# Performance work log

Measured on AMD Instinct MI355X. Metric: run time of the kernel, lower is better.

The kernel has to match this reference:

```python
import jax, jax.numpy as jnp
import numpy as np

DIM = 1024
HEADS = 16
HEAD_DIM = DIM // HEADS
D_FF = 4 * DIM
EPS = 1e-5


def _layernorm(x, g, b):
    mu = jnp.mean(x, axis=-1, keepdims=True)
    var = jnp.mean(jnp.square(x - mu), axis=-1, keepdims=True)
    return (x - mu) * jax.lax.rsqrt(var + EPS) * g + b


def setup_inputs() -> dict:
    key = jax.random.key(0)
    ks = jax.random.split(key, 8)
    s = 0.02
    return {
        "x": jax.random.normal(ks[0], (2, 2048, DIM), dtype=jnp.float32),
        "Wqkv": jax.random.normal(ks[1], (DIM, 3 * DIM), dtype=jnp.float32) * s,
        "bqkv": jnp.zeros((3 * DIM,), dtype=jnp.float32),
        "Wout": jax.random.normal(ks[2], (DIM, DIM), dtype=jnp.float32) * s,
        "bout": jnp.zeros((DIM,), dtype=jnp.float32),
        "W1": jax.random.normal(ks[3], (DIM, D_FF), dtype=jnp.float32) * s,
        "b1": jnp.zeros((D_FF,), dtype=jnp.float32),
        "W2": jax.random.normal(ks[4], (D_FF, DIM), dtype=jnp.float32) * s,
        "b2": jnp.zeros((DIM,), dtype=jnp.float32),
        "g1": jnp.ones((DIM,), dtype=jnp.float32),
        "be1": jnp.zeros((DIM,), dtype=jnp.float32),
        "g2": jnp.ones((DIM,), dtype=jnp.float32),
        "be2": jnp.zeros((DIM,), dtype=jnp.float32),
    }


def reference(x, Wqkv, bqkv, Wout, bout, W1, b1, W2, b2, g1, be1, g2, be2):
    B, T, C = x.shape
    # --- multi-head self-attention (explicit QK^T softmax, no mask/cache) ---
    qkv = (x @ Wqkv + bqkv).reshape(B, T, 3, HEADS, HEAD_DIM)
    q = qkv[:, :, 0].transpose(0, 2, 1, 3)  # (B,H,T,hd)
    k = qkv[:, :, 1].transpose(0, 2, 1, 3)
    v = qkv[:, :, 2].transpose(0, 2, 1, 3)
    scale = HEAD_DIM ** -0.5
    scores = jnp.einsum("bhqd,bhkd->bhqk", q, k) * scale  # (B,H,T,T)
    attn = jax.nn.softmax(scores, axis=-1)
    o = jnp.einsum("bhqk,bhkd->bhqd", attn, v)
    o = o.transpose(0, 2, 1, 3).reshape(B, T, C)
    attn_out = o @ Wout + bout
    # --- Post-LN: LN applied to sublayer output, then residual ---
    x = x + _layernorm(attn_out, g1, be1)
    # --- FFN with exact GELU ---
    h = jax.nn.gelu(x @ W1 + b1, approximate=False)
    ffn_out = h @ W2 + b2
    x = x + _layernorm(ffn_out, g2, be2)
    return x
```

## Files before the change

kernel.cpp:

```cpp
#include <hip/hip_runtime.h>
#include <cstdint>
#include <cstddef>

#define DIM 1024
#define HEADS 16
#define HD 64
#define DFF 4096
#define TSEQ 2048
#define EPS 1e-5f

#define WAITCNT_VM4 0xF74
#define WAITCNT_VM0 0xF70
#define WAITCNT_VM8 0xF78
#define WAITCNT_VM4_LGKM0 0x074
#define WAITCNT_VM0_LGKM0 0x070

typedef __bf16 bf16x8 __attribute__((ext_vector_type(8)));
typedef float floatx4 __attribute__((ext_vector_type(4)));

__device__ __forceinline__ unsigned short f2bf(float f) {
  union { float f; unsigned int u; } v; v.f = f;
  return (unsigned short)((v.u + 0x7FFFu + ((v.u >> 16) & 1u)) >> 16);
}

__device__ __forceinline__ float gelu_f(float v) {
  const float u = v * (0.7978845608f + 0.0356774081f * v * v);
  const float e = __expf(2.0f * u);
  const float t = 1.0f - 2.0f / (e + 1.0f);
  return 0.5f * v * (1.0f + t);
}

__device__ __forceinline__ void async16(const void* g, void* l) {
  __builtin_amdgcn_global_load_lds(
      (const __attribute__((address_space(1))) void*)g,
      (__attribute__((address_space(3))) void*)l, 16, 0, 0);
}

__global__ __launch_bounds__(256) void prep_all(const float* __restrict__ x,
                                                const float* __restrict__ Wqkv,
                                                const float* __restrict__ Wout,
                                                const float* __restrict__ W1,
                                                const float* __restrict__ W2,
                                                unsigned short* __restrict__ xb,
                                                unsigned short* __restrict__ WqkvT,
                                                unsigned short* __restrict__ WoutT,
                                                unsigned short* __restrict__ W1T,
                                                unsigned short* __restrict__ W2T) {
  const int bid = blockIdx.x;
  const int tid = threadIdx.x;
  if (bid < 4096) {
    const int i = bid * 256 + tid;
    float4 v = ((const float4*)x)[i];
    ushort4 o;
    o.x = f2bf(v.x); o.y = f2bf(v.y); o.z = f2bf(v.z); o.w = f2bf(v.w);
    ((ushort4*)xb)[i] = o;
    return;
  }
  int id = bid - 4096;
  const float* src; unsigned short* dst; int R, C, gx;
  if (id < 3072)      {            src = Wqkv; dst = WqkvT; R = 1024; C = 3072; gx = 96; }
  else if (id < 4096) { id -= 3072; src = Wout; dst = WoutT; R = 1024; C = 1024; gx = 32; }
  else if (id < 8192) { id -= 4096; src = W1;   dst = W1T;   R = 1024; C = 4096; gx = 128; }
  else                { id -= 8192; src = W2;   dst = W2T;   R = 4096; C = 1024; gx = 32; }
  const int c0 = (id % gx) * 32, r0 = (id / gx) * 32;
  const int tx = tid & 31, ty = tid >> 5;
  __shared__ float tile[32][33];
#pragma unroll
  for (int i = 0; i < 32; i += 8)
    tile[ty + i][tx] = src[(size_t)(r0 + ty + i) * C + c0 + tx];
  __syncthreads();
#pragma unroll
  for (int i = 0; i < 32; i += 8)
    dst[(size_t)(c0 + ty + i) * R + r0 + tx] = f2bf(tile[tx][ty + i]);
}

#define PIPELINED_KLOOP(NIT, STRIDE_EXPR)                                           \
  auto issue = [&](int s, int k0) {                                                  \
    async16(Ab0 + k0, &lds[s][tid * 8]);                                             \
    async16(Ab1 + k0, &lds[s][2048 + tid * 8]);                                      \
    async16(Bb0 + k0, &lds[s][4096 + tid * 8]);                                      \
    async16(Bb1 + k0, &lds[s][6144 + tid * 8]);                                      \
  };                                                                                 \
  issue(0, 0);                                                                       \
  issue(1, 32);                                                                      \
  int sidx = 0;                                                                      \
  for (int k = 0; k < (NIT); k++) {                                                  \
    if (k < (NIT)-1) __builtin_amdgcn_s_waitcnt(WAITCNT_VM4);                        \
    else             __builtin_amdgcn_s_waitcnt(WAITCNT_VM0);                        \
    __builtin_amdgcn_s_barrier();                                                    \
    if (k + 2 < (NIT)) {                                                             \
      int s2 = sidx + 2; if (s2 >= 3) s2 -= 3;                                       \
      issue(s2, (k + 2) * 32);                                                       \
    }                                                                                \
    bf16x8 af[4], bg[4];                                                             \
    _Pragma("unroll")                                                                \
    for (int mi = 0; mi < 4; mi++)                                                   \
      af[mi] = *(const bf16x8*)&lds[sidx][(wm + mi * 16 + l16) * 32 + quad * 8];     \
    _Pragma("unroll")                                                                \
    for (int ni = 0; ni < 4; ni++)                                                   \
      bg[ni] = *(const bf16x8*)&lds[sidx][4096 + (wn + ni * 16 + l16) * 32 + quad * 8]; \
    _Pragma("unroll")                                                                \
    for (int mi = 0; mi < 4; mi++)                                                   \
      _Pragma("unroll")                                                              \
      for (int ni = 0; ni < 4; ni++)                                                 \
        acc[mi][ni] =                                                                \
            __builtin_amdgcn_mfma_f32_16x16x32_bf16(af[mi], bg[ni], acc[mi][ni], 0, 0, 0); \
    sidx = (sidx == 2) ? 0 : sidx + 1;                                               \
  }

template <int EPI>
__global__ __launch_bounds__(256) void gemm_bt(const unsigned short* __restrict__ A,
                                               const unsigned short* __restrict__ Bt,
                                               const float* __restrict__ bias,
                                               void* __restrict__ Cout,
                                               int M, int N, int K) {
  __shared__ unsigned short lds[3][8192];
  const int tid = threadIdx.x;
  const int bm = blockIdx.y * 128, bn = blockIdx.x * 128;
  const int wave = tid >> 6, lane = tid & 63;
  const int l16 = lane & 15, quad = lane >> 4;
  const int wm = (wave >> 1) * 64, wn = (wave & 1) * 64;

  floatx4 acc[4][4] = {};

  const int srow = tid >> 2;
  const int scol = (tid & 3) * 8;

  const unsigned short* Ab0 = A + (size_t)(bm + srow) * K + scol;
  const unsigned short* Ab1 = A + (size_t)(bm + 64 + srow) * K + scol;
  const unsigned short* Bb0 = Bt + (size_t)(bn + srow) * K + scol;
  const unsigned short* Bb1 = Bt + (size_t)(bn + 64 + srow) * K + scol;

  const int nit = K >> 5;
  PIPELINED_KLOOP(nit, 32)
  __syncthreads();

  if (EPI == 0) {
#pragma unroll
    for (int ni = 0; ni < 4; ni++) {
      const int col = bn + wn + ni * 16 + l16;
      const float bv = bias[col];
#pragma unroll
      for (int mi = 0; mi < 4; mi++) {
        const int row0 = bm + wm + mi * 16 + quad * 4;
#pragma unroll
        for (int r = 0; r < 4; r++)
          ((float*)Cout)[(size_t)(row0 + r) * N + col] = acc[mi][ni][r] + bv;
      }
    }
  } else {
    unsigned short* eb = &lds[0][wave * 1152];
    float bvv[4];
#pragma unroll
    for (int ni = 0; ni < 4; ni++) bvv[ni] = bias[bn + wn + ni * 16 + l16];
    const int lrow = lane >> 2, ck = lane & 3;
#pragma unroll
    for (int mi = 0; mi < 4; mi++) {
#pragma unroll
      for (int ni = 0; ni < 4; ni++)
#pragma unroll
        for (int r = 0; r < 4; r++)
          eb[(quad * 4 + r) * 72 + ni * 16 + l16] =
              f2bf(gelu_f(acc[mi][ni][r] + bvv[ni]));
      __syncthreads();
      unsigned short* gp =
          (unsigned short*)Cout + (size_t)(bm + wm + mi * 16 + lrow) * N + bn + wn;
#pragma unroll
      for (int j = 0; j < 2; j++)
        *(uint4*)(gp + j * 32 + ck * 8) = *(const uint4*)&eb[lrow * 72 + j * 32 + ck * 8];
      __syncthreads();
    }
  }
}

__global__ __launch_bounds__(256) void gemm_splitk(const unsigned short* __restrict__ A,
                                                   const unsigned short* __restrict__ Bt,
                                                   float* __restrict__ Cp,
                                                   int M, int N, int Ktot, int Ksl) {
  __shared__ unsigned short lds[3][8192];
  const int tid = threadIdx.x;
  const int bm = blockIdx.y * 128, bn = blockIdx.x * 128;
  const int koff = blockIdx.z * Ksl;
  const int wave = tid >> 6, lane = tid & 63;
  const int l16 = lane & 15, quad = lane >> 4;
  const int wm = (wave >> 1) * 64, wn = (wave & 1) * 64;

  floatx4 acc[4][4] = {};

  const int srow = tid >> 2;
  const int scol = (tid & 3) * 8;

  const unsigned short* Ab0 = A + (size_t)(bm + srow) * Ktot + koff + scol;
  const unsigned short* Ab1 = A + (size_t)(bm + 64 + srow) * Ktot + koff + scol;
  const unsigned short* Bb0 = Bt + (size_t)(bn + srow) * Ktot + koff + scol;
  const unsigned short* Bb1 = Bt + (size_t)(bn + 64 + srow) * Ktot + koff + scol;

  const int nit = Ksl >> 5;
  PIPELINED_KLOOP(nit, 32)

  float* out = Cp + (size_t)blockIdx.z * M * (size_t)N;
#pragma unroll
  for (int ni = 0; ni < 4; ni++) {
    const int col = bn + wn + ni * 16 + l16;
#pragma unroll
    for (int mi = 0; mi < 4; mi++) {
      const int row0 = bm + wm + mi * 16 + quad * 4;
#pragma unroll
      for (int r = 0; r < 4; r++)
        out[(size_t)(row0 + r) * N + col] = acc[mi][ni][r];
    }
  }
}

__global__ __launch_bounds__(256) void gemm_qkv(const unsigned short* __restrict__ A,
                                                const unsigned short* __restrict__ Bt,
                                                const float* __restrict__ bias,
                                                unsigned short* __restrict__ Qg,
                                                unsigned short* __restrict__ Kg,
                                                unsigned short* __restrict__ Vtg) {
  const int K = 1024;
  __shared__ unsigned short lds[3][8192];
  const int tid = threadIdx.x;
  const int bm = blockIdx.y * 128, bn = blockIdx.x * 128;
  const int wave = tid >> 6, lane = tid & 63;
  const int l16 = lane & 15, quad = lane >> 4;
  const int wm = (wave >> 1) * 64, wn = (wave & 1) * 64;

  floatx4 acc[4][4] = {};

  const int srow = tid >> 2;
  const int scol = (tid & 3) * 8;

  const unsigned short* Ab0 = A + (size_t)(bm + srow) * K + scol;
  const unsigned short* Ab1 = A + (size_t)(bm + 64 + srow) * K + scol;
  const unsigned short* Bb0 = Bt + (size_t)(bn + srow) * K + scol;
  const unsigned short* Bb1 = Bt + (size_t)(bn + 64 + srow) * K + scol;

  const int nit = K >> 5;
  PIPELINED_KLOOP(nit, 32)

#pragma unroll
  for (int ni = 0; ni < 4; ni++) {
    const int col = bn + wn + ni * 16 + l16;
    const float bv = bias[col];
    const int sec = col >> 10;
    const int cc = col & 1023;
    const int hh = cc >> 6, dd = cc & 63;
#pragma unroll
    for (int mi = 0; mi < 4; mi++) {
      const int row0 = bm + wm + mi * 16 + quad * 4;
      const int b2 = row0 >> 11, tt0 = row0 & 2047;
      if (sec == 0) {
        unsigned short* q = Qg + ((size_t)(b2 * HEADS + hh) * TSEQ + tt0) * HD + dd;
#pragma unroll
        for (int r = 0; r < 4; r++)
          q[(size_t)r * HD] = f2bf((acc[mi][ni][r] + bv) * 0.125f);
      } else if (sec == 1) {
        unsigned short* k = Kg + ((size_t)(b2 * HEADS + hh) * TSEQ + tt0) * HD + dd;
#pragma unroll
        for (int r = 0; r < 4; r++)
          k[(size_t)r * HD] = f2bf(acc[mi][ni][r] + bv);
      } else {
        ushort4 o;
        o.x = f2bf(acc[mi][ni][0] + bv);
        o.y = f2bf(acc[mi][ni][1] + bv);
        o.z = f2bf(acc[mi][ni][2] + bv);
        o.w = f2bf(acc[mi][ni][3] + bv);
        *(ushort4*)(Vtg + ((size_t)(b2 * HEADS + hh) * HD + dd) * TSEQ + tt0) = o;
      }
    }
  }
}

__global__ __launch_bounds__(256) void attn_mfma(const unsigned short* __restrict__ Qg,
                                                 const unsigned short* __restrict__ Kg,
                                                 const unsigned short* __restrict__ Vtg,
                                                 unsigned short* __restrict__ ob) {
  __shared__ unsigned short QPs[128 * 64];
  __shared__ unsigned short Ks[3][64 * 64];
  __shared__ unsigned short Vs[3][64 * 64];
  const int qt = blockIdx.x, h = blockIdx.y, b = blockIdx.z;
  const int tid = threadIdx.x;
  const int w = tid >> 6, lane = tid & 63, l16 = lane & 15, quad = lane >> 4;

  const int r0 = tid >> 3;
  const int c0 = (tid & 7) ^ (r0 & 7);

  const char* Qbase = (const char*)(Qg + ((size_t)(b * HEADS + h) * TSEQ + qt * 128) * HD);
  const char* Kbase = (const char*)(Kg + (size_t)(b * HEADS + h) * TSEQ * HD);
  const char* Vbase = (const char*)(Vtg + (size_t)(b * HEADS + h) * HD * TSEQ);

  auto issueKV = [&](int s, int ch) {
    const size_t koff = (size_t)ch * 64;
#pragma unroll
    for (int i = 0; i < 2; i++) {
      async16(Kbase + (koff + r0 + i * 32) * 128 + c0 * 16,
              (char*)Ks[s] + (i * 256 + tid) * 16);
      async16(Vbase + (size_t)(r0 + i * 32) * (TSEQ * 2) + koff * 2 + c0 * 16,
              (char*)Vs[s] + (i * 256 + tid) * 16);
    }
  };

#pragma unroll
  for (int i = 0; i < 4; i++)
    async16(Qbase + (size_t)(r0 + i * 32) * 128 + c0 * 16, (char*)QPs + (i * 256 + tid) * 16);
  issueKV(0, 0);
  issueKV(1, 1);

  __builtin_amdgcn_s_waitcnt(WAITCNT_VM8);
  __builtin_amdgcn_s_barrier();

  bf16x8 qf[2][2];
#pragma unroll
  for (int mi = 0; mi < 2; mi++)
#pragma unroll
    for (int kt = 0; kt < 2; kt++) {
      const int row = w * 32 + mi * 16 + l16;
      qf[mi][kt] = *(const bf16x8*)((const char*)QPs + row * 128 +
                                    (((quad + 4 * kt) ^ (row & 7)) * 16));
    }

  union { unsigned short u[8]; bf16x8 b; } onesu;
#pragma unroll
  for (int j = 0; j < 8; j++) onesu.u[j] = 0x3F80;
  const bf16x8 ones = onesu.b;

  floatx4 oacc[2][5] = {};
  char* Pw = (char*)QPs + w * 4096;

  const int NC = TSEQ / 64;
  int sidx = 0;
  for (int ch = 0; ch < NC; ch++) {
    if (ch < NC - 1) __builtin_amdgcn_s_waitcnt(WAITCNT_VM4_LGKM0);
    else             __builtin_amdgcn_s_waitcnt(WAITCNT_VM0_LGKM0);
    __builtin_amdgcn_s_barrier();
    if (ch + 2 < NC) {
      int s2 = sidx + 2; if (s2 >= 3) s2 -= 3;
      issueKV(s2, ch + 2);
    }
    floatx4 sacc[2][4] = {};
#pragma unroll
    for (int kt = 0; kt < 2; kt++) {
#pragma unroll
      for (int ni = 0; ni < 4; ni++) {
        const int row = ni * 16 + l16;
        bf16x8 kf = *(const bf16x8*)((const char*)Ks[sidx] + row * 128 +
                                     (((quad + 4 * kt) ^ (row & 7)) * 16));
#pragma unroll
        for (int mi = 0; mi < 2; mi++)
          sacc[mi][ni] =
              __builtin_amdgcn_mfma_f32_16x16x32_bf16(qf[mi][kt], kf, sacc[mi][ni], 0, 0, 0);
      }
    }
#pragma unroll
    for (int mi = 0; mi < 2; mi++)
#pragma unroll
      for (int ni = 0; ni < 4; ni++)
#pragma unroll
        for (int r = 0; r < 4; r++) {
          const float p = __expf(sacc[mi][ni][r]);
          const unsigned int pu = __builtin_bit_cast(unsigned int, p);
          const int m = mi * 16 + quad * 4 + r;
          const int key = ni * 16 + l16;
          *((unsigned short*)(Pw + m * 128 + (((key >> 3) ^ (m & 7)) * 16) +
                              (key & 7) * 2)) = (unsigned short)(pu >> 16);
        }
#pragma unroll
    for (int kt = 0; kt < 2; kt++) {
      bf16x8 pf[2], vf[4];
#pragma unroll
      for (int mi = 0; mi < 2; mi++) {
        const int row = mi * 16 + l16;
        pf[mi] = *(const bf16x8*)(Pw + row * 128 + (((quad + 4 * kt) ^ (row & 7)) * 16));
      }
#pragma unroll
      for (int nj = 0; nj < 4; nj++) {
        const int vrow = nj * 16 + l16;
        vf[nj] = *(const bf16x8*)((const char*)Vs[sidx] + vrow * 128 +
                                  (((quad + 4 * kt) ^ (vrow & 7)) * 16));
      }
#pragma unroll
      for (int mi = 0; mi < 2; mi++) {
#pragma unroll
        for (int nj = 0; nj < 4; nj++)
          oacc[mi][nj] =
              __builtin_amdgcn_mfma_f32_16x16x32_bf16(pf[mi], vf[nj], oacc[mi][nj], 0, 0, 0);
        oacc[mi][4] =
            __builtin_amdgcn_mfma_f32_16x16x32_bf16(pf[mi], ones, oacc[mi][4], 0, 0, 0);
      }
    }
    sidx = (sidx == 2) ? 0 : sidx + 1;
  }

#pragma unroll
  for (int mi = 0; mi < 2; mi++)
#pragma unroll
    for (int r = 0; r < 4; r++) {
      const float inv = 1.0f / oacc[mi][4][r];
      const int t = qt * 128 + w * 32 + mi * 16 + quad * 4 + r;
      unsigned short* orow = ob + (size_t)(b * TSEQ + t) * DIM + h * HD + l16;
#pragma unroll
      for (int nj = 0; nj < 4; nj++)
        orow[nj * 16] = f2bf(oacc[mi][nj][r] * inv);
    }
}

template <int NP, int WBF>
__global__ __launch_bounds__(256) void add_ln_red(const float* __restrict__ xin,
                                                  const float* __restrict__ parts,
                                                  const float* __restrict__ bias,
                                                  const float* __restrict__ gw,
                                                  const float* __restrict__ bw,
                                                  float* __restrict__ xout,
                                                  unsigned short* __restrict__ xbf) {
  const size_t MN = (size_t)4096 * DIM;
  const int row = blockIdx.x;
  const int tid = threadIdx.x;
  const int c = tid * 4;
  const size_t base = (size_t)row * DIM;
  float4 v = *(const float4*)(parts + base + c);
#pragma unroll
  for (int p = 1; p < NP; p++) {
    float4 t = *(const float4*)(parts + p * MN + base + c);
    v.x += t.x; v.y += t.y; v.z += t.z; v.w += t.w;
  }
  float4 bb = *(const float4*)(bias + c);
  v.x += bb.x; v.y += bb.y; v.z += bb.z; v.w += bb.w;

  float s = v.x + v.y + v.z + v.w;
  float s2 = v.x * v.x + v.y * v.y + v.z * v.z + v.w * v.w;
#pragma unroll
  for (int off = 1; off < 64; off <<= 1) {
    s += __shfl_xor(s, off);
    s2 += __shfl_xor(s2, off);
  }
  __shared__ float rsum[4], rsq[4];
  if ((tid & 63) == 0) { rsum[tid >> 6] = s; rsq[tid >> 6] = s2; }
  __syncthreads();
  s = rsum[0] + rsum[1] + rsum[2] + rsum[3];
  s2 = rsq[0] + rsq[1] + rsq[2] + rsq[3];
  const float mu = s * (1.0f / DIM);
  const float var = s2 * (1.0f / DIM) - mu * mu;
  const float rstd = rsqrtf(var + EPS);
  float4 xv = *(const float4*)(xin + base + c);
  float4 gv = *(const float4*)(gw + c);
  float4 bv = *(const float4*)(bw + c);
  float4 o;
  o.x = xv.x + (v.x - mu) * rstd * gv.x + bv.x;
  o.y = xv.y + (v.y - mu) * rstd * gv.y + bv.y;
  o.z = xv.z + (v.z - mu) * rstd * gv.z + bv.z;
  o.w = xv.w + (v.w - mu) * rstd * gv.w + bv.w;
  *(float4*)(xout + base + c) = o;
  if (WBF) {
    ushort4 ob;
    ob.x = f2bf(o.x); ob.y = f2bf(o.y); ob.z = f2bf(o.z); ob.w = f2bf(o.w);
    *(ushort4*)(xbf + base + c) = ob;
  }
}

extern "C" void kernel_launch(void* const* d_in, const int* in_sizes, int n_in,
                              void* d_out, int out_size, void* d_ws, size_t ws_size,
                              hipStream_t stream) {
  const float* x    = (const float*)d_in[0];
  const float* Wqkv = (const float*)d_in[1];
  const float* bqkv = (const float*)d_in[2];
  const float* Wout = (const float*)d_in[3];
  const float* bout = (const float*)d_in[4];
  const float* W1   = (const float*)d_in[5];
  const float* b1   = (const float*)d_in[6];
  const float* W2   = (const float*)d_in[7];
  const float* b2   = (const float*)d_in[8];
  const float* g1   = (const float*)d_in[9];
  const float* be1  = (const float*)d_in[10];
  const float* g2   = (const float*)d_in[11];
  const float* be2  = (const float*)d_in[12];

  char* w = (char*)d_ws;
  const size_t MB = 1048576;
  unsigned short* xb     = (unsigned short*)(w + 0 * MB);
  unsigned short* WqkvT  = (unsigned short*)(w + 8 * MB);
  unsigned short* WoutT  = (unsigned short*)(w + 14 * MB);
  unsigned short* W1T    = (unsigned short*)(w + 16 * MB);
  unsigned short* W2T    = (unsigned short*)(w + 24 * MB);
  unsigned short* Qb     = (unsigned short*)(w + 32 * MB);
  unsigned short* Kb     = (unsigned short*)(w + 40 * MB);
  unsigned short* Vtb    = (unsigned short*)(w + 48 * MB);
  unsigned short* obuf   = (unsigned short*)(w + 64 * MB);
  float*          atno_p = (float*)(w + 72 * MB);
  float*          x1     = (float*)(w + 104 * MB);
  unsigned short* x1b    = (unsigned short*)(w + 120 * MB);
  unsigned short* hb     = (unsigned short*)(w + 128 * MB);
  float*          ffn_p  = (float*)(w + 32 * MB);

  prep_all<<<16384, 256, 0, stream>>>(x, Wqkv, Wout, W1, W2, xb, WqkvT, WoutT, W1T, W2T);

  gemm_qkv<<<dim3(24, 32), 256, 0, stream>>>(xb, WqkvT, bqkv, Qb, Kb, Vtb);
  attn_mfma<<<dim3(16, 16, 2), 256, 0, stream>>>(Qb, Kb, Vtb, obuf);
  gemm_splitk<<<dim3(8, 32, 2), 256, 0, stream>>>(obuf, WoutT, atno_p, 4096, 1024, 1024, 512);
  add_ln_red<2, 1><<<4096, 256, 0, stream>>>(x, atno_p, bout, g1, be1, x1, x1b);
  gemm_bt<1><<<dim3(32, 32), 256, 0, stream>>>(x1b, W1T, b1, hb, 4096, 4096, 1024);
  gemm_splitk<<<dim3(8, 32, 2), 256, 0, stream>>>(hb, W2T, ffn_p, 4096, 1024, 4096, 2048);
  add_ln_red<2, 0><<<4096, 256, 0, stream>>>(x1, ffn_p, b2, g2, be2, (float*)d_out, nullptr);
}
```

Baseline: 361.6 us.

## Shrink attention tiles to 64 queries, double-buffer KV, use exp2 with folded scale

The attention kernel now handles 64 query rows per block instead of 128, giving 1024 blocks. LDS usage drops by moving from triple to double buffering of K/V, which is meant to allow more blocks per CU (launch bounds set to 4). The log2(e) factor is folded into the Q scaling so the softmax can use the raw v_exp_f32 instruction, and the P scratch layout is rewritten with a new swizzle. The change also adds s_setprio around the MFMA sections, remaps block IDs so consecutive blocks land on different XCDs, and moves the next K/V prefetch after a trailing barrier. The risks are less K/V reuse per block, more total K/V loading, and an extra barrier in every chunk.

```diff
diff --git a/kernel.cpp b/kernel.cpp
--- a/kernel.cpp
+++ b/kernel.cpp
@@ -14,6 +14,7 @@
 #define WAITCNT_VM8 0xF78
 #define WAITCNT_VM4_LGKM0 0x074
 #define WAITCNT_VM0_LGKM0 0x070
+#define WAITCNT_LGKM0 0xC07F
 
 typedef __bf16 bf16x8 __attribute__((ext_vector_type(8)));
 typedef float floatx4 __attribute__((ext_vector_type(4)));
@@ -21,6 +22,16 @@
 __device__ __forceinline__ unsigned short f2bf(float f) {
   union { float f; unsigned int u; } v; v.f = f;
   return (unsigned short)((v.u + 0x7FFFu + ((v.u >> 16) & 1u)) >> 16);
+}
+
+__device__ __forceinline__ float exp2_fast(float x) {
+#if __has_builtin(__builtin_amdgcn_exp2f)
+  return __builtin_amdgcn_exp2f(x);
+#else
+  float r;
+  asm("v_exp_f32 %0, %1" : "=v"(r) : "v"(x));
+  return r;
+#endif
 }
 
 __device__ __forceinline__ float gelu_f(float v) {
@@ -239,6 +250,7 @@
   const int nit = K >> 5;
   PIPELINED_KLOOP(nit, 32)
 
+  const float QSCALE = 0.125f * 1.44269504089f;
 #pragma unroll
   for (int ni = 0; ni < 4; ni++) {
     const int col = bn + wn + ni * 16 + l16;
@@ -254,7 +266,7 @@
         unsigned short* q = Qg + ((size_t)(b2 * HEADS + hh) * TSEQ + tt0) * HD + dd;
 #pragma unroll
         for (int r = 0; r < 4; r++)
-          q[(size_t)r * HD] = f2bf((acc[mi][ni][r] + bv) * 0.125f);
+          q[(size_t)r * HD] = f2bf((acc[mi][ni][r] + bv) * QSCALE);
       } else if (sec == 1) {
         unsigned short* k = Kg + ((size_t)(b2 * HEADS + hh) * TSEQ + tt0) * HD + dd;
 #pragma unroll
@@ -272,21 +284,26 @@
   }
 }
 
-__global__ __launch_bounds__(256) void attn_mfma(const unsigned short* __restrict__ Qg,
-                                                 const unsigned short* __restrict__ Kg,
-                                                 const unsigned short* __restrict__ Vtg,
-                                                 unsigned short* __restrict__ ob) {
-  __shared__ unsigned short QPs[128 * 64];
-  __shared__ unsigned short Ks[3][64 * 64];
-  __shared__ unsigned short Vs[3][64 * 64];
-  const int qt = blockIdx.x, h = blockIdx.y, b = blockIdx.z;
+__global__ __launch_bounds__(256, 4) void attn_mfma(const unsigned short* __restrict__ Qg,
+                                                    const unsigned short* __restrict__ Kg,
+                                                    const unsigned short* __restrict__ Vtg,
+                                                    unsigned short* __restrict__ ob) {
+  __shared__ unsigned short QPs[64 * 64];
+  __shared__ unsigned short Ks[2][64 * 64];
+  __shared__ unsigned short Vs[2][64 * 64];
+
+  const int bid = blockIdx.x;
+  const int lid = (bid & 7) * 128 + (bid >> 3);
+  const int qt = lid & 31;
+  const int h = (lid >> 5) & 15;
+  const int b = lid >> 9;
   const int tid = threadIdx.x;
   const int w = tid >> 6, lane = tid & 63, l16 = lane & 15, quad = lane >> 4;
 
   const int r0 = tid >> 3;
   const int c0 = (tid & 7) ^ (r0 & 7);
 
-  const char* Qbase = (const char*)(Qg + ((size_t)(b * HEADS + h) * TSEQ + qt * 128) * HD);
+  const char* Qbase = (const char*)(Qg + ((size_t)(b * HEADS + h) * TSEQ + qt * 64) * HD);
   const char* Kbase = (const char*)(Kg + (size_t)(b * HEADS + h) * TSEQ * HD);
   const char* Vbase = (const char*)(Vtg + (size_t)(b * HEADS + h) * HD * TSEQ);
 
@@ -302,7 +319,7 @@
   };
 
 #pragma unroll
-  for (int i = 0; i < 4; i++)
+  for (int i = 0; i < 2; i++)
     async16(Qbase + (size_t)(r0 + i * 32) * 128 + c0 * 16, (char*)QPs + (i * 256 + tid) * 16);
   issueKV(0, 0);
   issueKV(1, 1);
@@ -310,99 +327,88 @@
   __builtin_amdgcn_s_waitcnt(WAITCNT_VM8);
   __builtin_amdgcn_s_barrier();
 
-  bf16x8 qf[2][2];
-#pragma unroll
-  for (int mi = 0; mi < 2; mi++)
-#pragma unroll
-    for (int kt = 0; kt < 2; kt++) {
-      const int row = w * 32 + mi * 16 + l16;
-      qf[mi][kt] = *(const bf16x8*)((const char*)QPs + row * 128 +
-                                    (((quad + 4 * kt) ^ (row & 7)) * 16));
-    }
+  bf16x8 qf[2];
+  {
+    const int row = w * 16 + l16;
+#pragma unroll
+    for (int kt = 0; kt < 2; kt++)
+      qf[kt] = *(const bf16x8*)((const char*)QPs + row * 128 +
+                                (((quad + 4 * kt) ^ (row & 7)) * 16));
+  }
 
   union { unsigned short u[8]; bf16x8 b; } onesu;
 #pragma unroll
   for (int j = 0; j < 8; j++) onesu.u[j] = 0x3F80;
   const bf16x8 ones = onesu.b;
 
-  floatx4 oacc[2][5] = {};
-  char* Pw = (char*)QPs + w * 4096;
+  floatx4 oacc[5] = {};
+  char* PwC = (char*)QPs + w * 2048;
+  const int pbase = quad * 512 + ((quad & 1) << 6) + ((l16 >> 3) << 4) + (l16 & 7) * 2;
 
   const int NC = TSEQ / 64;
   int sidx = 0;
   for (int ch = 0; ch < NC; ch++) {
-    if (ch < NC - 1) __builtin_amdgcn_s_waitcnt(WAITCNT_VM4_LGKM0);
-    else             __builtin_amdgcn_s_waitcnt(WAITCNT_VM0_LGKM0);
+    if (ch < NC - 1) __builtin_amdgcn_s_waitcnt(WAITCNT_VM4);
+    else             __builtin_amdgcn_s_waitcnt(WAITCNT_VM0);
     __builtin_amdgcn_s_barrier();
-    if (ch + 2 < NC) {
-      int s2 = sidx + 2; if (s2 >= 3) s2 -= 3;
-      issueKV(s2, ch + 2);
-    }
-    floatx4 sacc[2][4] = {};
+
+    floatx4 sacc[4] = {};
+    __builtin_amdgcn_s_setprio(1);
 #pragma unroll
     for (int kt = 0; kt < 2; kt++) {
 #pragma unroll
       for (int ni = 0; ni < 4; ni++) {
-        const int row = ni * 16 + l16;
-        bf16x8 kf = *(const bf16x8*)((const char*)Ks[sidx] + row * 128 +
-                                     (((quad + 4 * kt) ^ (row & 7)) * 16));
-#pragma unroll
-        for (int mi = 0; mi < 2; mi++)
-          sacc[mi][ni] =
-              __builtin_amdgcn_mfma_f32_16x16x32_bf16(qf[mi][kt], kf, sacc[mi][ni], 0, 0, 0);
+        const int krow = ni * 16 + l16;
+        bf16x8 kf = *(const bf16x8*)((const char*)Ks[sidx] + krow * 128 +
+                                     (((quad + 4 * kt) ^ (krow & 7)) * 16));
+        sacc[ni] =
+            __builtin_amdgcn_mfma_f32_16x16x32_bf16(qf[kt], kf, sacc[ni], 0, 0, 0);
       }
     }
-#pragma unroll
-    for (int mi = 0; mi < 2; mi++)
-#pragma unroll
-      for (int ni = 0; ni < 4; ni++)
-#pragma unroll
-        for (int r = 0; r < 4; r++) {
-          const float p = __expf(sacc[mi][ni][r]);
-          const unsigned int pu = __builtin_bit_cast(unsigned int, p);
-          const int m = mi * 16 + quad * 4 + r;
-          const int key = ni * 16 + l16;
-          *((unsigned short*)(Pw + m * 128 + (((key >> 3) ^ (m & 7)) * 16) +
-                              (key & 7) * 2)) = (unsigned short)(pu >> 16);
-        }
+    __builtin_amdgcn_s_setprio(0);
+
+#pragma unroll
+    for (int ni = 0; ni < 4; ni++)
+#pragma unroll
+      for (int r = 0; r < 4; r++) {
+        const float p = exp2_fast(sacc[ni][r]);
+        const unsigned int pu = __builtin_bit_cast(unsigned int, p);
+        *((unsigned short*)(PwC +
+                            (pbase ^ (r * 128 + (((ni << 1) ^ r) << 4))))) =
+            (unsigned short)(pu >> 16);
+      }
+
+    __builtin_amdgcn_s_setprio(1);
 #pragma unroll
     for (int kt = 0; kt < 2; kt++) {
-      bf16x8 pf[2], vf[4];
-#pragma unroll
-      for (int mi = 0; mi < 2; mi++) {
-        const int row = mi * 16 + l16;
-        pf[mi] = *(const bf16x8*)(Pw + row * 128 + (((quad + 4 * kt) ^ (row & 7)) * 16));
-      }
+      bf16x8 pf = *(const bf16x8*)(PwC + l16 * 128 +
+                                   (((quad + 4 * kt) ^ (l16 & 7)) * 16));
 #pragma unroll
       for (int nj = 0; nj < 4; nj++) {
         const int vrow = nj * 16 + l16;
-        vf[nj] = *(const bf16x8*)((const char*)Vs[sidx] + vrow * 128 +
-                                  (((quad + 4 * kt) ^ (vrow & 7)) * 16));
+        bf16x8 vf = *(const bf16x8*)((const char*)Vs[sidx] + vrow * 128 +
+                                     (((quad + 4 * kt) ^ (vrow & 7)) * 16));
+        oacc[nj] = __builtin_amdgcn_mfma_f32_16x16x32_bf16(pf, vf, oacc[nj], 0, 0, 0);
       }
-#pragma unroll
-      for (int mi = 0; mi < 2; mi++) {
-#pragma unroll
-        for (int nj = 0; nj < 4; nj++)
-          oacc[mi][nj] =
-              __builtin_amdgcn_mfma_f32_16x16x32_bf16(pf[mi], vf[nj], oacc[mi][nj], 0, 0, 0);
-        oacc[mi][4] =
-            __builtin_amdgcn_mfma_f32_16x16x32_bf16(pf[mi], ones, oacc[mi][4], 0, 0, 0);
-      }
-    }
-    sidx = (sidx == 2) ? 0 : sidx + 1;
-  }
-
-#pragma unroll
-  for (int mi = 0; mi < 2; mi++)
-#pragma unroll
-    for (int r = 0; r < 4; r++) {
-      const float inv = 1.0f / oacc[mi][4][r];
-      const int t = qt * 128 + w * 32 + mi * 16 + quad * 4 + r;
-      unsigned short* orow = ob + (size_t)(b * TSEQ + t) * DIM + h * HD + l16;
-#pragma unroll
-      for (int nj = 0; nj < 4; nj++)
-        orow[nj * 16] = f2bf(oacc[mi][nj][r] * inv);
-    }
+      oacc[4] = __builtin_amdgcn_mfma_f32_16x16x32_bf16(pf, ones, oacc[4], 0, 0, 0);
+    }
+    __builtin_amdgcn_s_setprio(0);
+
+    __builtin_amdgcn_s_waitcnt(WAITCNT_LGKM0);
+    __builtin_amdgcn_s_barrier();
+    if (ch + 2 < NC) issueKV(sidx, ch + 2);
+    sidx ^= 1;
+  }
+
+#pragma unroll
+  for (int r = 0; r < 4; r++) {
+    const float inv = 1.0f / oacc[4][r];
+    const int t = qt * 64 + w * 16 + quad * 4 + r;
+    unsigned short* orow = ob + (size_t)(b * TSEQ + t) * DIM + h * HD + l16;
+#pragma unroll
+    for (int nj = 0; nj < 4; nj++)
+      orow[nj * 16] = f2bf(oacc[nj][r] * inv);
+  }
 }
 
 template <int NP, int WBF>
@@ -495,7 +501,7 @@
   prep_all<<<16384, 256, 0, stream>>>(x, Wqkv, Wout, W1, W2, xb, WqkvT, WoutT, W1T, W2T);
 
   gemm_qkv<<<dim3(24, 32), 256, 0, stream>>>(xb, WqkvT, bqkv, Qb, Kb, Vtb);
-  attn_mfma<<<dim3(16, 16, 2), 256, 0, stream>>>(Qb, Kb, Vtb, obuf);
+  attn_mfma<<<1024, 256, 0, stream>>>(Qb, Kb, Vtb, obuf);
   gemm_splitk<<<dim3(8, 32, 2), 256, 0, stream>>>(obuf, WoutT, atno_p, 4096, 1024, 1024, 512);
   add_ln_red<2, 1><<<4096, 256, 0, stream>>>(x, atno_p, bout, g1, be1, x1, x1b);
   gemm_bt<1><<<dim3(32, 32), 256, 0, stream>>>(x1b, W1T, b1, hb, 4096, 4096, 1024);
```

New measurement: 349.8 us. 1.03x faster.
